# Performance work log

Hardware: AMD Instinct MI355X
Metric: run time of the kernel (lower is better)

The kernel has to match this reference:

```python
import jax, jax.numpy as jnp
import numpy as np

V, E, H, B, L_ENC, T = 32000, 512, 512, 32, 512, 64


def setup_inputs() -> dict:
    key = jax.random.key(0)
    ks = jax.random.split(key, 15)
    s = 0.05  # weight scale to keep activations in a sane range
    return {
        "x": jax.random.randint(ks[0], (B, 1), 0, V),
        "encod_out": jax.random.normal(ks[1], (B, L_ENC, H), jnp.float32),
        "h": jax.random.normal(ks[2], (1, B, H), jnp.float32) * s,
        "c": jax.random.normal(ks[3], (1, B, H), jnp.float32) * s,
        "targets": jax.random.randint(ks[4], (B, T), 0, V),
        "mask_att": jax.random.randint(ks[5], (B, L_ENC), 0, 2).astype(jnp.int32),
        "teacher_forcing_ratio": 1,
        "embed_table": jax.random.normal(ks[6], (V, E), jnp.float32) * s,
        "W_ih": jax.random.normal(ks[7], (4 * H, E + H), jnp.float32) * s,
        "W_hh": jax.random.normal(ks[8], (4 * H, H), jnp.float32) * s,
        "b_ih": jax.random.normal(ks[9], (4 * H,), jnp.float32) * s,
        "b_hh": jax.random.normal(ks[10], (4 * H,), jnp.float32) * s,
        "W_out": jax.random.normal(ks[11], (V, H), jnp.float32) * s,
        "b_out": jax.random.normal(ks[12], (V,), jnp.float32) * s,
        "mask_logit": jax.random.randint(ks[13], (V,), 0, 2).astype(bool),
    }


def reference(x, encod_out, h, c, targets, mask_att, teacher_forcing_ratio,
              embed_table, W_ih, W_hh, b_ih, b_hh, W_out, b_out, mask_logit):
    # Eval-mode (dropout = identity), teacher forcing ratio = 1.0 (always teacher),
    # num_layers = 1 LSTM. torch LSTM gate order: i, f, g, o.
    neg_inf = jnp.float32(-jnp.inf)
    att_masked = (mask_att == 0)              # (B, L_enc) True -> mask out
    bias = b_ih + b_hh                         # (4H,)
    # Teacher-forced input tokens per step: [x[:,0], targets[:,0..T-2]]
    toks = jnp.concatenate([x[:, :1], targets[:, :-1]], axis=1).T  # (T, B)

    def step(carry, tok):
        hs, cs = carry                          # (B, H) each
        emb = embed_table[tok]                  # (B, E)
        # dot-product attention with last-layer hidden as query
        scores = jnp.einsum('blh,bh->bl', encod_out, hs)      # (B, L_enc)
        scores = jnp.where(att_masked, neg_inf, scores)
        w = jax.nn.softmax(scores, axis=-1)
        ctx = jnp.einsum('bl,blh->bh', w, encod_out)          # (B, H)
        # single-step LSTM cell
        xin = jnp.concatenate([emb, ctx], axis=-1)            # (B, E+H)
        gates = xin @ W_ih.T + hs @ W_hh.T + bias             # (B, 4H)
        i, f, g, o = jnp.split(gates, 4, axis=-1)
        cn = jax.nn.sigmoid(f) * cs + jax.nn.sigmoid(i) * jnp.tanh(g)
        hn = jax.nn.sigmoid(o) * jnp.tanh(cn)
        logit = hn @ W_out.T + b_out                          # (B, V)
        logit = jnp.where(mask_logit, neg_inf, logit)
        return (hn, cn), logit

    (_, _), logits = jax.lax.scan(step, (h[0], c[0]), toks)   # logits: (T, B, V)
    return jnp.transpose(logits, (1, 0, 2))                   # (B, T, V)
```

## Files before the change

kernel.cpp:

```cpp
#include <hip/hip_runtime.h>

#define V_ 32000
#define E_ 512
#define H_ 512
#define B_ 32
#define L_ 512
#define T_ 64
#define G4 2048
#define KX 1024

typedef __attribute__((ext_vector_type(8))) short short8;
typedef __attribute__((ext_vector_type(4))) float f32x4;

#define NEG_INF (-__builtin_inff())
#define MASK_SENTINEL (-1.0e30f)

__device__ __forceinline__ unsigned short f2bf(float f) {
  unsigned int u = __float_as_uint(f);
  u += 0x7fffu + ((u >> 16) & 1u);
  return (unsigned short)(u >> 16);
}
__device__ __forceinline__ float sigmoidf_(float x) { return 1.f / (1.f + expf(-x)); }


__global__ __launch_bounds__(256) void k_cast_wout(const float* __restrict__ W,
                                                   unsigned short* __restrict__ Wb) {
  size_t i = ((size_t)blockIdx.x * 256 + threadIdx.x) * 8;
  float4 a = *(const float4*)(W + i);
  float4 b = *(const float4*)(W + i + 4);
  unsigned short r[8] = {f2bf(a.x), f2bf(a.y), f2bf(a.z), f2bf(a.w),
                         f2bf(b.x), f2bf(b.y), f2bf(b.z), f2bf(b.w)};
  *(uint4*)(Wb + i) = *(uint4*)r;
}

__global__ __launch_bounds__(256) void k_pack(const float* __restrict__ Wih, const float* __restrict__ Whh,
                                              const float* __restrict__ bih, const float* __restrict__ bhh,
                                              const float* __restrict__ h0, const float* __restrict__ c0,
                                              unsigned short* __restrict__ WihE, unsigned short* __restrict__ WcH,
                                              float* __restrict__ biasp, float* __restrict__ hf,
                                              float* __restrict__ cf, unsigned short* __restrict__ xin) {
  int bid = blockIdx.x;
  if (bid < G4) {
    int p = bid;
    int j = p >> 5, c = p & 31;
    int ni = c >> 4, g = (c >> 2) & 3, r4 = c & 3;
    int G = g * 512 + j * 8 + ni * 4 + r4;
    for (int k = threadIdx.x; k < KX; k += 256) {
      float w = (k < 512) ? Wih[(size_t)G * 1024 + 512 + k] : Whh[(size_t)G * 512 + (k - 512)];
      WcH[(size_t)p * KX + k] = f2bf(w);
    }
    for (int k = threadIdx.x; k < 512; k += 256)
      WihE[(size_t)p * 512 + k] = f2bf(Wih[(size_t)G * 1024 + k]);
    if (threadIdx.x == 0) biasp[p] = bih[G] + bhh[G];
  } else {
    int b = bid - G4;
    for (int k = threadIdx.x; k < 512; k += 256) {
      float hv = h0[b * 512 + k];
      hf[b * 512 + k] = hv;
      cf[b * 512 + k] = c0[b * 512 + k];
      xin[b * KX + 512 + k] = f2bf(hv);
    }
  }
}

__global__ __launch_bounds__(256) void k_emb(const int* __restrict__ x, const int* __restrict__ targ,
                                             const float* __restrict__ etab, unsigned short* __restrict__ Emb) {
  int m = blockIdx.x;
  int t = m >> 5, b = m & 31;
  int tok = (t == 0) ? x[b] : targ[b * T_ + (t - 1)];
  const float* row = etab + (size_t)tok * E_;
  for (int k = threadIdx.x; k < E_; k += 256)
    Emb[(size_t)m * E_ + k] = f2bf(row[k]);
}

template <int MODE>
__global__ __launch_bounds__(256) void k_gemm128(const unsigned short* __restrict__ A,
                                                 const unsigned short* __restrict__ Bm, int K,
                                                 const float* __restrict__ bias,
                                                 const unsigned char* __restrict__ mask,
                                                 float* __restrict__ C) {
  __shared__ unsigned short As[128 * 32];
  __shared__ unsigned short Bs[128 * 32];
  int tid = threadIdx.x;
  int wave = tid >> 6, lane = tid & 63;
  int wm = wave >> 1, wn = wave & 1;
  int n0 = blockIdx.x * 128, m0 = blockIdx.y * 128;
  int lr = tid >> 2;
  int lc = (tid & 3) * 8;
  int q = lane >> 4, fr = lane & 15;
  f32x4 acc[4][4] = {};
  for (int kk = 0; kk < K; kk += 32) {
    *(uint4*)&As[lr * 32 + lc]        = *(const uint4*)&A[(size_t)(m0 + lr) * K + kk + lc];
    *(uint4*)&As[(lr + 64) * 32 + lc] = *(const uint4*)&A[(size_t)(m0 + lr + 64) * K + kk + lc];
    *(uint4*)&Bs[lr * 32 + lc]        = *(const uint4*)&Bm[(size_t)(n0 + lr) * K + kk + lc];
    *(uint4*)&Bs[(lr + 64) * 32 + lc] = *(const uint4*)&Bm[(size_t)(n0 + lr + 64) * K + kk + lc];
    __syncthreads();
    short8 af[4], bf[4];
#pragma unroll
    for (int i = 0; i < 4; i++) af[i] = *(short8*)&As[(wm * 64 + i * 16 + fr) * 32 + q * 8];
#pragma unroll
    for (int jj = 0; jj < 4; jj++) bf[jj] = *(short8*)&Bs[(wn * 64 + jj * 16 + fr) * 32 + q * 8];
#pragma unroll
    for (int i = 0; i < 4; i++)
#pragma unroll
      for (int jj = 0; jj < 4; jj++)
        acc[i][jj] = __builtin_amdgcn_mfma_f32_16x16x32_bf16(af[i], bf[jj], acc[i][jj], 0, 0, 0);
    __syncthreads();
  }
#pragma unroll
  for (int i = 0; i < 4; i++)
#pragma unroll
    for (int jj = 0; jj < 4; jj++) {
      int col = n0 + wn * 64 + jj * 16 + fr;
#pragma unroll
      for (int e = 0; e < 4; e++) {
        int row = m0 + wm * 64 + i * 16 + q * 4 + e;
        float v = acc[i][jj][e];
        if (MODE == 0) {
          C[(size_t)row * G4 + col] = v + bias[col];
        } else {
          float val = v + bias[col];
          if (mask[col]) val = MASK_SENTINEL;
          int t = row >> 5, b = row & 31;
          C[((size_t)b * T_ + t) * V_ + col] = val;
        }
      }
    }
}


__global__ __launch_bounds__(256) void k_att1(const float* __restrict__ enc, const int* __restrict__ matt,
                                              const float* __restrict__ hf, float* __restrict__ ctxp,
                                              float* __restrict__ mS) {
  __shared__ float h_s[512];
  __shared__ float sc_s[32];
  __shared__ float w_s[32];
  __shared__ float red_s[4 * 512];
  int bid = blockIdx.x;
  int b = bid >> 4, ch = bid & 15;
  int tid = threadIdx.x, wave = tid >> 6, lane = tid & 63;
  h_s[tid] = hf[b * 512 + tid];
  h_s[tid + 256] = hf[b * 512 + tid + 256];
  __syncthreads();
  int l0 = ch * 32 + wave * 8;
  float a_reg[8][8];
#pragma unroll
  for (int r = 0; r < 8; r++) {
    const float* row = enc + ((size_t)(b * L_ + l0 + r)) * H_;
    float s = 0.f;
#pragma unroll
    for (int i = 0; i < 8; i++) {
      float av = row[lane + i * 64];
      a_reg[r][i] = av;
      s += av * h_s[lane + i * 64];
    }
#pragma unroll
    for (int off = 32; off; off >>= 1) s += __shfl_xor(s, off, 64);
    if (matt[b * L_ + l0 + r] == 0) s = NEG_INF;
    if (lane == 0) sc_s[wave * 8 + r] = s;
  }
  __syncthreads();
  float m = NEG_INF;
#pragma unroll
  for (int i = 0; i < 32; i++) m = fmaxf(m, sc_s[i]);
  float wv[8];
#pragma unroll
  for (int r = 0; r < 8; r++) {
    float s = sc_s[wave * 8 + r];
    wv[r] = (m == NEG_INF) ? 0.f : expf(s - m);
    if (lane == 0) w_s[wave * 8 + r] = wv[r];
  }
  float cpart[8];
#pragma unroll
  for (int i = 0; i < 8; i++) cpart[i] = 0.f;
#pragma unroll
  for (int r = 0; r < 8; r++)
#pragma unroll
    for (int i = 0; i < 8; i++) cpart[i] += wv[r] * a_reg[r][i];
#pragma unroll
  for (int i = 0; i < 8; i++) red_s[wave * 512 + lane + i * 64] = cpart[i];
  __syncthreads();
  for (int jv = tid; jv < 512; jv += 256) {
    float s4 = red_s[jv] + red_s[512 + jv] + red_s[1024 + jv] + red_s[1536 + jv];
    ctxp[(size_t)bid * 512 + jv] = s4;
  }
  if (tid == 0) {
    float S = 0.f;
#pragma unroll
    for (int i = 0; i < 32; i++) S += w_s[i];
    mS[bid * 2] = m;
    mS[bid * 2 + 1] = S;
  }
}

__global__ __launch_bounds__(256) void k_att2(const float* __restrict__ ctxp, const float* __restrict__ mS,
                                              unsigned short* __restrict__ xin) {
  int b = blockIdx.x, tid = threadIdx.x;
  float m = NEG_INF;
#pragma unroll
  for (int k = 0; k < 16; k++) m = fmaxf(m, mS[(b * 16 + k) * 2]);
  float coef[16];
  float S = 0.f;
#pragma unroll
  for (int k = 0; k < 16; k++) {
    float mk = mS[(b * 16 + k) * 2];
    float ck = (mk == NEG_INF || m == NEG_INF) ? 0.f : expf(mk - m);
    coef[k] = ck;
    S += ck * mS[(b * 16 + k) * 2 + 1];
  }
  float inv = (S > 0.f) ? 1.f / S : 0.f;
  for (int jv = tid; jv < 512; jv += 256) {
    float a = 0.f;
#pragma unroll
    for (int k = 0; k < 16; k++) a += coef[k] * ctxp[((size_t)(b * 16 + k)) * 512 + jv];
    xin[b * KX + jv] = f2bf(a * inv);
  }
}

__global__ __launch_bounds__(256) void k_gates(const unsigned short* __restrict__ xin,
                                               const unsigned short* __restrict__ WcH,
                                               const float* __restrict__ preg, float* __restrict__ hf,
                                               float* __restrict__ cf, unsigned short* __restrict__ xinh,
                                               unsigned short* __restrict__ Hn, int t) {
  __shared__ float g_s[32 * 32];
  int j = blockIdx.x;
  int tid = threadIdx.x, wave = tid >> 6, lane = tid & 63;
  int mi = wave & 1, ni = wave >> 1;
  int q = lane >> 4, fr = lane & 15;
  f32x4 acc = {};
  const unsigned short* Aptr = xin + (size_t)(mi * 16 + fr) * KX + q * 8;
  const unsigned short* Bptr = WcH + (size_t)(j * 32 + ni * 16 + fr) * KX + q * 8;
  for (int kk = 0; kk < KX; kk += 32) {
    short8 af = *(const short8*)(Aptr + kk);
    short8 bfv = *(const short8*)(Bptr + kk);
    acc = __builtin_amdgcn_mfma_f32_16x16x32_bf16(af, bfv, acc, 0, 0, 0);
  }
#pragma unroll
  for (int e = 0; e < 4; e++) {
    int brow = mi * 16 + q * 4 + e;
    int c = ni * 16 + fr;
    g_s[brow * 32 + c] = acc[e] + preg[((size_t)(t * B_ + brow)) * G4 + j * 32 + c];
  }
  __syncthreads();
  int b = tid >> 3, r = tid & 7;
  int ni2 = r >> 2, r4 = r & 3;
  float iv = g_s[b * 32 + ni2 * 16 + 0 * 4 + r4];
  float fv = g_s[b * 32 + ni2 * 16 + 1 * 4 + r4];
  float gv = g_s[b * 32 + ni2 * 16 + 2 * 4 + r4];
  float ov = g_s[b * 32 + ni2 * 16 + 3 * 4 + r4];
  int hcol = j * 8 + r;
  float cold = cf[b * 512 + hcol];
  float cn = sigmoidf_(fv) * cold + sigmoidf_(iv) * tanhf(gv);
  float hn = sigmoidf_(ov) * tanhf(cn);
  cf[b * 512 + hcol] = cn;
  hf[b * 512 + hcol] = hn;
  unsigned short hb = f2bf(hn);
  xinh[b * KX + 512 + hcol] = hb;
  Hn[((size_t)(t * B_ + b)) * H_ + hcol] = hb;
}


extern "C" void kernel_launch(void* const* d_in, const int* in_sizes, int n_in, void* d_out,
                              int out_size, void* d_ws, size_t ws_size, hipStream_t stream) {
  const int* x = (const int*)d_in[0];
  const float* enc = (const float*)d_in[1];
  const float* h0 = (const float*)d_in[2];
  const float* c0 = (const float*)d_in[3];
  const int* targ = (const int*)d_in[4];
  const int* matt = (const int*)d_in[5];
  const float* etab = (const float*)d_in[7];
  const float* Wih = (const float*)d_in[8];
  const float* Whh = (const float*)d_in[9];
  const float* bih = (const float*)d_in[10];
  const float* bhh = (const float*)d_in[11];
  const float* Wout = (const float*)d_in[12];
  const float* bout = (const float*)d_in[13];
  const unsigned char* mlog = (const unsigned char*)d_in[14];
  float* out = (float*)d_out;

  char* ws = (char*)d_ws;
  size_t o = 0;
  unsigned short* Woutb = (unsigned short*)(ws + o); o += (size_t)V_ * H_ * 2;
  unsigned short* Emb   = (unsigned short*)(ws + o); o += (size_t)T_ * B_ * E_ * 2;
  unsigned short* WihE  = (unsigned short*)(ws + o); o += (size_t)G4 * E_ * 2;
  unsigned short* WcH   = (unsigned short*)(ws + o); o += (size_t)G4 * KX * 2;
  float* preg           = (float*)(ws + o);          o += (size_t)T_ * B_ * G4 * 4;
  float* biasp          = (float*)(ws + o);          o += (size_t)G4 * 4;
  float* hf             = (float*)(ws + o);          o += (size_t)B_ * H_ * 4;
  float* cf             = (float*)(ws + o);          o += (size_t)B_ * H_ * 4;
  unsigned short* xin   = (unsigned short*)(ws + o); o += (size_t)B_ * KX * 2;
  float* ctxp           = (float*)(ws + o);          o += (size_t)B_ * 16 * H_ * 4;
  float* mS             = (float*)(ws + o);          o += (size_t)B_ * 16 * 2 * 4;
  unsigned short* Hn    = (unsigned short*)(ws + o); o += (size_t)T_ * B_ * H_ * 2;

  hipLaunchKernelGGL(k_cast_wout, dim3((V_ * H_) / (256 * 8)), dim3(256), 0, stream, Wout, Woutb);
  hipLaunchKernelGGL(k_pack, dim3(G4 + B_), dim3(256), 0, stream, Wih, Whh, bih, bhh, h0, c0, WihE,
                     WcH, biasp, hf, cf, xin);
  hipLaunchKernelGGL(k_emb, dim3(T_ * B_), dim3(256), 0, stream, x, targ, etab, Emb);
  hipLaunchKernelGGL((k_gemm128<0>), dim3(G4 / 128, (T_ * B_) / 128), dim3(256), 0, stream, Emb,
                     WihE, E_, biasp, (const unsigned char*)nullptr, preg);
  for (int t = 0; t < T_; t++) {
    hipLaunchKernelGGL(k_att1, dim3(B_ * 16), dim3(256), 0, stream, enc, matt, hf, ctxp, mS);
    hipLaunchKernelGGL(k_att2, dim3(B_), dim3(256), 0, stream, ctxp, mS, xin);
    hipLaunchKernelGGL(k_gates, dim3(64), dim3(256), 0, stream, xin, WcH, preg, hf, cf, xin, Hn, t);
  }
  hipLaunchKernelGGL((k_gemm128<1>), dim3(V_ / 128, (T_ * B_) / 128), dim3(256), 0, stream, Hn,
                     Woutb, H_, bout, mlog, out);
}
```

Baseline: 1.992 ms.

## Fuse recurrent loop into persistent kernel with atomic-counter inter-workgroup sync

Replaces the 192 per-step launches (attention partial, attention combine, gates) with one persistent kernel of 224 workgroups. Stages hand off through global atomic counters with acquire/release spin-waits instead of kernel boundaries. The encoder output is pre-cast to fp16 and scored with fdot2, and fast __expf is used, which reduces precision. The goal is to remove launch overhead and halve encoder bandwidth, at the cost of relying on all 224 workgroups being co-resident and on spin-wait latency.

```diff
diff --git a/kernel.cpp b/kernel.cpp
--- a/kernel.cpp
+++ b/kernel.cpp
@@ -11,6 +11,8 @@
 
 typedef __attribute__((ext_vector_type(8))) short short8;
 typedef __attribute__((ext_vector_type(4))) float f32x4;
+typedef __attribute__((ext_vector_type(2))) _Float16 half2v;
+typedef __attribute__((ext_vector_type(4))) _Float16 half4v;
 
 #define NEG_INF (-__builtin_inff())
 #define MASK_SENTINEL (-1.0e30f)
@@ -20,7 +22,29 @@
   u += 0x7fffu + ((u >> 16) & 1u);
   return (unsigned short)(u >> 16);
 }
-__device__ __forceinline__ float sigmoidf_(float x) { return 1.f / (1.f + expf(-x)); }
+__device__ __forceinline__ float sigmoidf_(float x) { return 1.f / (1.f + __expf(-x)); }
+
+__device__ __forceinline__ float dot2f(half2v a, half2v b, float c) {
+#if __has_builtin(__builtin_amdgcn_fdot2)
+  return __builtin_amdgcn_fdot2(a, b, c, false);
+#else
+  return c + (float)a[0] * (float)b[0] + (float)a[1] * (float)b[1];
+#endif
+}
+
+__device__ __forceinline__ void wg_wait(unsigned* cnt, unsigned target) {
+  if (threadIdx.x == 0) {
+    while (__hip_atomic_load(cnt, __ATOMIC_ACQUIRE, __HIP_MEMORY_SCOPE_AGENT) < target)
+      __builtin_amdgcn_s_sleep(2);
+  }
+  __syncthreads();
+}
+__device__ __forceinline__ void wg_post(unsigned* cnt) {
+  __threadfence();
+  __syncthreads();
+  if (threadIdx.x == 0)
+    __hip_atomic_fetch_add(cnt, 1u, __ATOMIC_RELEASE, __HIP_MEMORY_SCOPE_AGENT);
+}
 
 
 __global__ __launch_bounds__(256) void k_cast_wout(const float* __restrict__ W,
@@ -33,12 +57,21 @@
   *(uint4*)(Wb + i) = *(uint4*)r;
 }
 
+__global__ __launch_bounds__(256) void k_cast_enc(const float* __restrict__ E,
+                                                  _Float16* __restrict__ E2) {
+  size_t i = ((size_t)blockIdx.x * 256 + threadIdx.x) * 4;
+  float4 a = *(const float4*)(E + i);
+  half4v r = {(_Float16)a.x, (_Float16)a.y, (_Float16)a.z, (_Float16)a.w};
+  *(half4v*)(E2 + i) = r;
+}
+
 __global__ __launch_bounds__(256) void k_pack(const float* __restrict__ Wih, const float* __restrict__ Whh,
                                               const float* __restrict__ bih, const float* __restrict__ bhh,
                                               const float* __restrict__ h0, const float* __restrict__ c0,
                                               unsigned short* __restrict__ WihE, unsigned short* __restrict__ WcH,
                                               float* __restrict__ biasp, float* __restrict__ hf,
-                                              float* __restrict__ cf, unsigned short* __restrict__ xin) {
+                                              float* __restrict__ cf, unsigned short* __restrict__ xin,
+                                              unsigned* __restrict__ cnts) {
   int bid = blockIdx.x;
   if (bid < G4) {
     int p = bid;
@@ -52,7 +85,7 @@
     for (int k = threadIdx.x; k < 512; k += 256)
       WihE[(size_t)p * 512 + k] = f2bf(Wih[(size_t)G * 1024 + k]);
     if (threadIdx.x == 0) biasp[p] = bih[G] + bhh[G];
-  } else {
+  } else if (bid < G4 + B_) {
     int b = bid - G4;
     for (int k = threadIdx.x; k < 512; k += 256) {
       float hv = h0[b * 512 + k];
@@ -60,6 +93,8 @@
       cf[b * 512 + k] = c0[b * 512 + k];
       xin[b * KX + 512 + k] = f2bf(hv);
     }
+  } else {
+    for (int k = threadIdx.x; k < 34 * 16; k += 256) cnts[k] = 0u;
   }
 }
 
@@ -128,135 +163,147 @@
     }
 }
 
-
-__global__ __launch_bounds__(256) void k_att1(const float* __restrict__ enc, const int* __restrict__ matt,
-                                              const float* __restrict__ hf, float* __restrict__ ctxp,
-                                              float* __restrict__ mS) {
-  __shared__ float h_s[512];
-  __shared__ float sc_s[32];
-  __shared__ float w_s[32];
-  __shared__ float red_s[4 * 512];
-  int bid = blockIdx.x;
-  int b = bid >> 4, ch = bid & 15;
-  int tid = threadIdx.x, wave = tid >> 6, lane = tid & 63;
-  h_s[tid] = hf[b * 512 + tid];
-  h_s[tid + 256] = hf[b * 512 + tid + 256];
-  __syncthreads();
-  int l0 = ch * 32 + wave * 8;
-  float a_reg[8][8];
-#pragma unroll
-  for (int r = 0; r < 8; r++) {
-    const float* row = enc + ((size_t)(b * L_ + l0 + r)) * H_;
-    float s = 0.f;
-#pragma unroll
-    for (int i = 0; i < 8; i++) {
-      float av = row[lane + i * 64];
-      a_reg[r][i] = av;
-      s += av * h_s[lane + i * 64];
-    }
-#pragma unroll
-    for (int off = 32; off; off >>= 1) s += __shfl_xor(s, off, 64);
-    if (matt[b * L_ + l0 + r] == 0) s = NEG_INF;
-    if (lane == 0) sc_s[wave * 8 + r] = s;
+__global__ __launch_bounds__(256, 1) void k_rec(
+    const _Float16* __restrict__ enc2, const int* __restrict__ matt,
+    const float* __restrict__ c0p, const unsigned short* __restrict__ WcH,
+    const float* __restrict__ preg, float* __restrict__ hf,
+    unsigned short* __restrict__ xin, unsigned short* __restrict__ Hn,
+    float* __restrict__ ctxp, float* __restrict__ mS, unsigned* __restrict__ cnts) {
+  int wg = blockIdx.x, tid = threadIdx.x;
+  unsigned* cntB = cnts + 32 * 16;
+  unsigned* cnt3 = cnts + 33 * 16;
+
+  if (wg < 128) {
+    int b = wg >> 2, q = wg & 3;
+    int wave = tid >> 6, lane = tid & 63;
+    __shared__ float red[4][512];
+    __shared__ float scw[128];
+    __shared__ float mred[4], sred[4];
+    __shared__ _Float16 h2s[512];
+    const _Float16* encb = enc2 + (size_t)(b * L_ + q * 128 + wave * 32) * H_;
+    unsigned* cntA = cnts + b * 16;
+    int mreg = 1;
+    if (lane < 32) mreg = matt[b * L_ + q * 128 + wave * 32 + lane];
+    for (int t = 0; t < T_; t++) {
+      wg_wait(cnt3, 64u * (unsigned)t);
+      h2s[tid] = (_Float16)hf[b * 512 + tid];
+      h2s[tid + 256] = (_Float16)hf[b * 512 + 256 + tid];
+      __syncthreads();
+      half2v hr[4];
+#pragma unroll
+      for (int k = 0; k < 4; k++) hr[k] = *(half2v*)&h2s[lane * 8 + k * 2];
+      half2v areg[32][4];
+      float mloc = NEG_INF;
+#pragma unroll
+      for (int l = 0; l < 32; l++) {
+        const half2v* rp = (const half2v*)(encb + (size_t)l * H_ + lane * 8);
+        float s = 0.f;
+#pragma unroll
+        for (int k = 0; k < 4; k++) {
+          areg[l][k] = rp[k];
+          s = dot2f(areg[l][k], hr[k], s);
+        }
+#pragma unroll
+        for (int off = 32; off; off >>= 1) s += __shfl_xor(s, off, 64);
+        if (__shfl(mreg, l, 64) == 0) s = NEG_INF;
+        if (lane == 0) scw[wave * 32 + l] = s;
+        mloc = fmaxf(mloc, s);
+      }
+      if (lane == 0) mred[wave] = mloc;
+      __syncthreads();
+      float m_wg = fmaxf(fmaxf(mred[0], mred[1]), fmaxf(mred[2], mred[3]));
+      float Sl = 0.f;
+      float cp[8] = {0.f, 0.f, 0.f, 0.f, 0.f, 0.f, 0.f, 0.f};
+#pragma unroll
+      for (int l = 0; l < 32; l++) {
+        float s = scw[wave * 32 + l];
+        float w = (m_wg == NEG_INF) ? 0.f : __expf(s - m_wg);
+        Sl += w;
+#pragma unroll
+        for (int k = 0; k < 4; k++) {
+          cp[k * 2]     += w * (float)areg[l][k][0];
+          cp[k * 2 + 1] += w * (float)areg[l][k][1];
+        }
+      }
+      if (lane == 0) sred[wave] = Sl;
+#pragma unroll
+      for (int k = 0; k < 8; k++) red[wave][lane * 8 + k] = cp[k];
+      __syncthreads();
+      for (int h = tid; h < 512; h += 256) {
+        float v = red[0][h] + red[1][h] + red[2][h] + red[3][h];
+        ctxp[(size_t)(b * 4 + q) * 512 + h] = v;
+      }
+      if (tid == 0) {
+        mS[(b * 4 + q) * 2] = m_wg;
+        mS[(b * 4 + q) * 2 + 1] = sred[0] + sred[1] + sred[2] + sred[3];
+      }
+      wg_post(cntA);
+    }
+  } else if (wg < 160) {
+    int b = wg - 128;
+    unsigned* cntA = cnts + b * 16;
+    for (int t = 0; t < T_; t++) {
+      wg_wait(cntA, 4u * (unsigned)(t + 1));
+      float m0 = mS[(b * 4 + 0) * 2], m1 = mS[(b * 4 + 1) * 2];
+      float m2 = mS[(b * 4 + 2) * 2], m3 = mS[(b * 4 + 3) * 2];
+      float M = fmaxf(fmaxf(m0, m1), fmaxf(m2, m3));
+      float k0 = (M == NEG_INF || m0 == NEG_INF) ? 0.f : __expf(m0 - M);
+      float k1 = (M == NEG_INF || m1 == NEG_INF) ? 0.f : __expf(m1 - M);
+      float k2 = (M == NEG_INF || m2 == NEG_INF) ? 0.f : __expf(m2 - M);
+      float k3 = (M == NEG_INF || m3 == NEG_INF) ? 0.f : __expf(m3 - M);
+      float S = k0 * mS[(b * 4 + 0) * 2 + 1] + k1 * mS[(b * 4 + 1) * 2 + 1] +
+                k2 * mS[(b * 4 + 2) * 2 + 1] + k3 * mS[(b * 4 + 3) * 2 + 1];
+      float inv = (S > 0.f) ? 1.f / S : 0.f;
+      for (int h = tid; h < 512; h += 256) {
+        float v = (k0 * ctxp[(size_t)(b * 4 + 0) * 512 + h] +
+                   k1 * ctxp[(size_t)(b * 4 + 1) * 512 + h] +
+                   k2 * ctxp[(size_t)(b * 4 + 2) * 512 + h] +
+                   k3 * ctxp[(size_t)(b * 4 + 3) * 512 + h]) * inv;
+        xin[b * KX + h] = f2bf(v);
+      }
+      wg_post(cntB);
+    }
+  } else {
+    int j = wg - 160;
+    int wave = tid >> 6, lane = tid & 63;
+    int mi = wave & 1, ni = wave >> 1;
+    int qq = lane >> 4, fr = lane & 15;
+    __shared__ float g_s[32 * 32];
+    int bb = tid >> 3, rr = tid & 7;
+    int hcol = j * 8 + rr;
+    float c_reg = c0p[bb * 512 + hcol];
+    const unsigned short* Aptr = xin + (size_t)(mi * 16 + fr) * KX + qq * 8;
+    const unsigned short* Bptr = WcH + (size_t)(j * 32 + ni * 16 + fr) * KX + qq * 8;
+    for (int t = 0; t < T_; t++) {
+      wg_wait(cntB, 32u * (unsigned)(t + 1));
+      f32x4 acc = {};
+      for (int kk = 0; kk < KX; kk += 32) {
+        short8 af = *(const short8*)(Aptr + kk);
+        short8 bfv = *(const short8*)(Bptr + kk);
+        acc = __builtin_amdgcn_mfma_f32_16x16x32_bf16(af, bfv, acc, 0, 0, 0);
+      }
+#pragma unroll
+      for (int e = 0; e < 4; e++) {
+        int brow = mi * 16 + qq * 4 + e;
+        int c = ni * 16 + fr;
+        g_s[brow * 32 + c] = acc[e] + preg[((size_t)(t * B_ + brow)) * G4 + j * 32 + c];
+      }
+      __syncthreads();
+      int ni2 = rr >> 2, r4 = rr & 3;
+      float iv = g_s[bb * 32 + ni2 * 16 + 0 * 4 + r4];
+      float fv = g_s[bb * 32 + ni2 * 16 + 1 * 4 + r4];
+      float gv = g_s[bb * 32 + ni2 * 16 + 2 * 4 + r4];
+      float ov = g_s[bb * 32 + ni2 * 16 + 3 * 4 + r4];
+      float cn = sigmoidf_(fv) * c_reg + sigmoidf_(iv) * tanhf(gv);
+      float hn = sigmoidf_(ov) * tanhf(cn);
+      c_reg = cn;
+      hf[bb * 512 + hcol] = hn;
+      unsigned short hb = f2bf(hn);
+      xin[bb * KX + 512 + hcol] = hb;
+      Hn[((size_t)(t * B_ + bb)) * H_ + hcol] = hb;
+      wg_post(cnt3);
+    }
   }
-  __syncthreads();
-  float m = NEG_INF;
-#pragma unroll
-  for (int i = 0; i < 32; i++) m = fmaxf(m, sc_s[i]);
-  float wv[8];
-#pragma unroll
-  for (int r = 0; r < 8; r++) {
-    float s = sc_s[wave * 8 + r];
-    wv[r] = (m == NEG_INF) ? 0.f : expf(s - m);
-    if (lane == 0) w_s[wave * 8 + r] = wv[r];
-  }
-  float cpart[8];
-#pragma unroll
-  for (int i = 0; i < 8; i++) cpart[i] = 0.f;
-#pragma unroll
-  for (int r = 0; r < 8; r++)
-#pragma unroll
-    for (int i = 0; i < 8; i++) cpart[i] += wv[r] * a_reg[r][i];
-#pragma unroll
-  for (int i = 0; i < 8; i++) red_s[wave * 512 + lane + i * 64] = cpart[i];
-  __syncthreads();
-  for (int jv = tid; jv < 512; jv += 256) {
-    float s4 = red_s[jv] + red_s[512 + jv] + red_s[1024 + jv] + red_s[1536 + jv];
-    ctxp[(size_t)bid * 512 + jv] = s4;
-  }
-  if (tid == 0) {
-    float S = 0.f;
-#pragma unroll
-    for (int i = 0; i < 32; i++) S += w_s[i];
-    mS[bid * 2] = m;
-    mS[bid * 2 + 1] = S;
-  }
-}
-
-__global__ __launch_bounds__(256) void k_att2(const float* __restrict__ ctxp, const float* __restrict__ mS,
-                                              unsigned short* __restrict__ xin) {
-  int b = blockIdx.x, tid = threadIdx.x;
-  float m = NEG_INF;
-#pragma unroll
-  for (int k = 0; k < 16; k++) m = fmaxf(m, mS[(b * 16 + k) * 2]);
-  float coef[16];
-  float S = 0.f;
-#pragma unroll
-  for (int k = 0; k < 16; k++) {
-    float mk = mS[(b * 16 + k) * 2];
-    float ck = (mk == NEG_INF || m == NEG_INF) ? 0.f : expf(mk - m);
-    coef[k] = ck;
-    S += ck * mS[(b * 16 + k) * 2 + 1];
-  }
-  float inv = (S > 0.f) ? 1.f / S : 0.f;
-  for (int jv = tid; jv < 512; jv += 256) {
-    float a = 0.f;
-#pragma unroll
-    for (int k = 0; k < 16; k++) a += coef[k] * ctxp[((size_t)(b * 16 + k)) * 512 + jv];
-    xin[b * KX + jv] = f2bf(a * inv);
-  }
-}
-
-__global__ __launch_bounds__(256) void k_gates(const unsigned short* __restrict__ xin,
-                                               const unsigned short* __restrict__ WcH,
-                                               const float* __restrict__ preg, float* __restrict__ hf,
-                                               float* __restrict__ cf, unsigned short* __restrict__ xinh,
-                                               unsigned short* __restrict__ Hn, int t) {
-  __shared__ float g_s[32 * 32];
-  int j = blockIdx.x;
-  int tid = threadIdx.x, wave = tid >> 6, lane = tid & 63;
-  int mi = wave & 1, ni = wave >> 1;
-  int q = lane >> 4, fr = lane & 15;
-  f32x4 acc = {};
-  const unsigned short* Aptr = xin + (size_t)(mi * 16 + fr) * KX + q * 8;
-  const unsigned short* Bptr = WcH + (size_t)(j * 32 + ni * 16 + fr) * KX + q * 8;
-  for (int kk = 0; kk < KX; kk += 32) {
-    short8 af = *(const short8*)(Aptr + kk);
-    short8 bfv = *(const short8*)(Bptr + kk);
-    acc = __builtin_amdgcn_mfma_f32_16x16x32_bf16(af, bfv, acc, 0, 0, 0);
-  }
-#pragma unroll
-  for (int e = 0; e < 4; e++) {
-    int brow = mi * 16 + q * 4 + e;
-    int c = ni * 16 + fr;
-    g_s[brow * 32 + c] = acc[e] + preg[((size_t)(t * B_ + brow)) * G4 + j * 32 + c];
-  }
-  __syncthreads();
-  int b = tid >> 3, r = tid & 7;
-  int ni2 = r >> 2, r4 = r & 3;
-  float iv = g_s[b * 32 + ni2 * 16 + 0 * 4 + r4];
-  float fv = g_s[b * 32 + ni2 * 16 + 1 * 4 + r4];
-  float gv = g_s[b * 32 + ni2 * 16 + 2 * 4 + r4];
-  float ov = g_s[b * 32 + ni2 * 16 + 3 * 4 + r4];
-  int hcol = j * 8 + r;
-  float cold = cf[b * 512 + hcol];
-  float cn = sigmoidf_(fv) * cold + sigmoidf_(iv) * tanhf(gv);
-  float hn = sigmoidf_(ov) * tanhf(cn);
-  cf[b * 512 + hcol] = cn;
-  hf[b * 512 + hcol] = hn;
-  unsigned short hb = f2bf(hn);
-  xinh[b * KX + 512 + hcol] = hb;
-  Hn[((size_t)(t * B_ + b)) * H_ + hcol] = hb;
 }
 
 
@@ -289,21 +336,21 @@
   float* hf             = (float*)(ws + o);          o += (size_t)B_ * H_ * 4;
   float* cf             = (float*)(ws + o);          o += (size_t)B_ * H_ * 4;
   unsigned short* xin   = (unsigned short*)(ws + o); o += (size_t)B_ * KX * 2;
-  float* ctxp           = (float*)(ws + o);          o += (size_t)B_ * 16 * H_ * 4;
-  float* mS             = (float*)(ws + o);          o += (size_t)B_ * 16 * 2 * 4;
+  float* ctxp           = (float*)(ws + o);          o += (size_t)B_ * 4 * H_ * 4;
+  float* mS             = (float*)(ws + o);          o += (size_t)B_ * 4 * 2 * 4;
   unsigned short* Hn    = (unsigned short*)(ws + o); o += (size_t)T_ * B_ * H_ * 2;
+  _Float16* enc2        = (_Float16*)(ws + o);       o += (size_t)B_ * L_ * H_ * 2;
+  unsigned* cnts        = (unsigned*)(ws + o);       o += 34 * 16 * 4;
 
   hipLaunchKernelGGL(k_cast_wout, dim3((V_ * H_) / (256 * 8)), dim3(256), 0, stream, Wout, Woutb);
-  hipLaunchKernelGGL(k_pack, dim3(G4 + B_), dim3(256), 0, stream, Wih, Whh, bih, bhh, h0, c0, WihE,
-                     WcH, biasp, hf, cf, xin);
+  hipLaunchKernelGGL(k_cast_enc, dim3((B_ * L_ * H_) / (256 * 4)), dim3(256), 0, stream, enc, enc2);
+  hipLaunchKernelGGL(k_pack, dim3(G4 + B_ + 1), dim3(256), 0, stream, Wih, Whh, bih, bhh, h0, c0,
+                     WihE, WcH, biasp, hf, cf, xin, cnts);
   hipLaunchKernelGGL(k_emb, dim3(T_ * B_), dim3(256), 0, stream, x, targ, etab, Emb);
   hipLaunchKernelGGL((k_gemm128<0>), dim3(G4 / 128, (T_ * B_) / 128), dim3(256), 0, stream, Emb,
                      WihE, E_, biasp, (const unsigned char*)nullptr, preg);
-  for (int t = 0; t < T_; t++) {
-    hipLaunchKernelGGL(k_att1, dim3(B_ * 16), dim3(256), 0, stream, enc, matt, hf, ctxp, mS);
-    hipLaunchKernelGGL(k_att2, dim3(B_), dim3(256), 0, stream, ctxp, mS, xin);
-    hipLaunchKernelGGL(k_gates, dim3(64), dim3(256), 0, stream, xin, WcH, preg, hf, cf, xin, Hn, t);
-  }
+  hipLaunchKernelGGL(k_rec, dim3(224), dim3(256), 0, stream, enc2, matt, c0, WcH, preg, hf, xin,
+                     Hn, ctxp, mS, cnts);
   hipLaunchKernelGGL((k_gemm128<1>), dim3(V_ / 128, (T_ * B_) / 128), dim3(256), 0, stream, Hn,
                      Woutb, H_, bout, mlog, out);
 }
```

After: 6.112 ms. 207% more time.
